# Kernel tuning notes

Measured on AMD Instinct MI355X. Metric: run time of the kernel, lower is better.

Reference implementation:

```python
import jax, jax.numpy as jnp
import numpy as np

SQ, SK, B, H, D = 2048, 2048, 2, 16, 64
LAYER_NUMBER = 1  # coeff for query_key_layer_scaling
MASK_FILL = -10000.0  # attention_mask_func fill value


def setup_inputs() -> dict:
    key = jax.random.key(0)
    kq, kk, kv = jax.random.split(key, 3)
    query_layer = jax.random.normal(kq, (SQ, B, H, D), dtype=jnp.float32)
    key_layer = jax.random.normal(kk, (SK, B, H, D), dtype=jnp.float32)
    value_layer = jax.random.normal(kv, (SK, B, H, D), dtype=jnp.float32)
    attention_mask = jnp.zeros((B, 1, SQ, SK), dtype=bool)  # ignored for causal mask type
    return {
        "query_layer": query_layer,
        "key_layer": key_layer,
        "value_layer": value_layer,
        "attention_mask": attention_mask,
    }


def reference(query_layer, key_layer, value_layer, attention_mask):
    sq, b, h, d = query_layer.shape
    sk = key_layer.shape[0]
    coeff = float(LAYER_NUMBER)
    norm_factor = np.sqrt(d) * coeff  # norm_factor = sqrt(d) * layer_number

    # BMM1: [b,h,sq,sk] scores, scaled by 1/norm_factor
    scores = jnp.einsum("sbhd,tbhd->bhst", query_layer, key_layer) / norm_factor

    # FusedScaleMaskSoftmax: scale by coeff in fp32, causal mask, softmax
    scores = scores.astype(jnp.float32) * coeff
    causal = jnp.triu(jnp.ones((sq, sk), dtype=bool), k=1)  # True above diagonal -> masked
    scores = jnp.where(causal[None, None], MASK_FILL, scores)
    probs = jax.nn.softmax(scores, axis=-1).astype(query_layer.dtype)

    # dropout p=0.0 -> identity

    # BMM2: context [sq,b,h,d] -> [sq,b,h*d]
    context = jnp.einsum("bhst,tbhd->sbhd", probs, value_layer)
    return context.reshape(sq, b, h * d)
```

## Files before the change

### kernel.cpp

```cpp
#include <hip/hip_runtime.h>

typedef short bf16x8 __attribute__((ext_vector_type(8)));
typedef float f32x4 __attribute__((ext_vector_type(4)));
typedef unsigned u32x4 __attribute__((ext_vector_type(4)));
typedef unsigned u32x2 __attribute__((ext_vector_type(2)));

#define RS 2048
#define LDSK 72
#define QSCALE 0.18033688011f

static __device__ __forceinline__ unsigned pkbf(float a, float b) {
    union { float f; unsigned u; } ua, ub; ua.f = a; ub.f = b;
    return ((ua.u + 0x8000u) >> 16) | ((ub.u + 0x8000u) & 0xffff0000u);
}

static __device__ __forceinline__ float fexp2(float x) {
#if __has_builtin(__builtin_amdgcn_exp2f)
    return __builtin_amdgcn_exp2f(x);
#else
    return exp2f(x);
#endif
}

__global__ __launch_bounds__(256, 2)
void fa_fwd(const float* __restrict__ Q, const float* __restrict__ K,
            const float* __restrict__ V, float* __restrict__ Out)
{
    __shared__ short Ksh[64 * LDSK];
    __shared__ short Vt[64 * LDSK];
    __shared__ short Psh[4][16 * LDSK];

    const int x = blockIdx.x;
    const int bh = blockIdx.y;
    const int base = bh * 64;
    const int tid = threadIdx.x;
    const int wave = tid >> 6, lane = tid & 63;
    const int n15 = lane & 15, quad = lane >> 4;

    const int tA = x;
    const int tB = 31 - x;

    const int krow = tid >> 2, kcg = (tid & 3) * 16;
    const int vkey = (tid & 31) * 2, vd = (tid >> 5) * 4;

    bf16x8 qfA[2], qfB[2];
    {
        const float* qa = Q + (size_t)(tA * 64 + wave * 16 + n15) * RS + base + quad * 8;
        const float* qb = Q + (size_t)(tB * 64 + wave * 16 + n15) * RS + base + quad * 8;
        #pragma unroll
        for (int ks = 0; ks < 2; ++ks) {
            f32x4 a0 = *(const f32x4*)(qa + ks * 32) * QSCALE;
            f32x4 a1 = *(const f32x4*)(qa + ks * 32 + 4) * QSCALE;
            union { u32x4 u; bf16x8 s; } wa;
            wa.u[0] = pkbf(a0[0], a0[1]); wa.u[1] = pkbf(a0[2], a0[3]);
            wa.u[2] = pkbf(a1[0], a1[1]); wa.u[3] = pkbf(a1[2], a1[3]);
            qfA[ks] = wa.s;
            f32x4 b0 = *(const f32x4*)(qb + ks * 32) * QSCALE;
            f32x4 b1 = *(const f32x4*)(qb + ks * 32 + 4) * QSCALE;
            union { u32x4 u; bf16x8 s; } wb;
            wb.u[0] = pkbf(b0[0], b0[1]); wb.u[1] = pkbf(b0[2], b0[3]);
            wb.u[2] = pkbf(b1[0], b1[1]); wb.u[3] = pkbf(b1[2], b1[3]);
            qfB[ks] = wb.s;
        }
    }

    f32x4 OA[4], OB[4];
    #pragma unroll
    for (int i = 0; i < 4; ++i) { OA[i] = (f32x4){0.f,0.f,0.f,0.f}; OB[i] = (f32x4){0.f,0.f,0.f,0.f}; }
    float lA = 0.f, lB = 0.f;

    f32x4 rk0, rk1, rk2, rk3, rv0, rv1, rv2, rv3;

    auto prefetch = [&](int kt) {
        const int kb = kt * 64;
        const float* kp = K + (size_t)(kb + krow) * RS + base + kcg;
        rk0 = *(const f32x4*)kp;       rk1 = *(const f32x4*)(kp + 4);
        rk2 = *(const f32x4*)(kp + 8); rk3 = *(const f32x4*)(kp + 12);
        const float* vp = V + (size_t)(kb + vkey) * RS + base + vd;
        rv0 = *(const f32x4*)vp;        rv1 = *(const f32x4*)(vp + RS);
        rv2 = *(const f32x4*)(vp + 32); rv3 = *(const f32x4*)(vp + RS + 32);
    };

    auto stage = [&]() {
        u32x4 w0; w0[0] = pkbf(rk0[0], rk0[1]); w0[1] = pkbf(rk0[2], rk0[3]);
                  w0[2] = pkbf(rk1[0], rk1[1]); w0[3] = pkbf(rk1[2], rk1[3]);
        *(u32x4*)&Ksh[krow * LDSK + kcg] = w0;
        u32x4 w1; w1[0] = pkbf(rk2[0], rk2[1]); w1[1] = pkbf(rk2[2], rk2[3]);
                  w1[2] = pkbf(rk3[0], rk3[1]); w1[3] = pkbf(rk3[2], rk3[3]);
        *(u32x4*)&Ksh[krow * LDSK + kcg + 8] = w1;
        #pragma unroll
        for (int i = 0; i < 4; ++i) {
            *(unsigned*)&Vt[(vd + i) * LDSK + vkey] = pkbf(rv0[i], rv1[i]);
            *(unsigned*)&Vt[(vd + 32 + i) * LDSK + vkey] = pkbf(rv2[i], rv3[i]);
        }
    };

    auto compute = [&](int tbase, int kb, bool diag, const bf16x8* qf, f32x4* O, float& l) {
        f32x4 S[4];
        #pragma unroll
        for (int mb = 0; mb < 4; ++mb) {
            f32x4 s = (f32x4){0.f,0.f,0.f,0.f};
            bf16x8 kf0 = *(const bf16x8*)&Ksh[(mb * 16 + n15) * LDSK + quad * 8];
            s = __builtin_amdgcn_mfma_f32_16x16x32_bf16(kf0, qf[0], s, 0, 0, 0);
            bf16x8 kf1 = *(const bf16x8*)&Ksh[(mb * 16 + n15) * LDSK + 32 + quad * 8];
            s = __builtin_amdgcn_mfma_f32_16x16x32_bf16(kf1, qf[1], s, 0, 0, 0);
            S[mb] = s;
        }
        if (diag) {
            int q = tbase + wave * 16 + n15;
            #pragma unroll
            for (int mb = 0; mb < 4; ++mb)
                #pragma unroll
                for (int r = 0; r < 4; ++r)
                    if (kb + mb * 16 + quad * 4 + r > q) S[mb][r] = -1e30f;
        }
        float rs = 0.f;
        #pragma unroll
        for (int mb = 0; mb < 4; ++mb) {
            float p0 = fexp2(S[mb][0]), p1 = fexp2(S[mb][1]);
            float p2 = fexp2(S[mb][2]), p3 = fexp2(S[mb][3]);
            rs += (p0 + p1) + (p2 + p3);
            u32x2 w; w[0] = pkbf(p0, p1); w[1] = pkbf(p2, p3);
            *(u32x2*)&Psh[wave][n15 * LDSK + mb * 16 + quad * 4] = w;
        }
        rs += __shfl_xor(rs, 16);
        rs += __shfl_xor(rs, 32);
        l += rs;
        bf16x8 pf0 = *(const bf16x8*)&Psh[wave][n15 * LDSK + quad * 8];
        bf16x8 pf1 = *(const bf16x8*)&Psh[wave][n15 * LDSK + 32 + quad * 8];
        #pragma unroll
        for (int db = 0; db < 4; ++db) {
            bf16x8 vf0 = *(const bf16x8*)&Vt[(db * 16 + n15) * LDSK + quad * 8];
            O[db] = __builtin_amdgcn_mfma_f32_16x16x32_bf16(pf0, vf0, O[db], 0, 0, 0);
            bf16x8 vf1 = *(const bf16x8*)&Vt[(db * 16 + n15) * LDSK + 32 + quad * 8];
            O[db] = __builtin_amdgcn_mfma_f32_16x16x32_bf16(pf1, vf1, O[db], 0, 0, 0);
        }
    };

    prefetch(0);
    const int ktmax = tB;
    for (int kt = 0; kt <= ktmax; ++kt) {
        __syncthreads();
        stage();
        __syncthreads();
        if (kt < ktmax) prefetch(kt + 1);
        compute(tB * 64, kt * 64, kt == tB, qfB, OB, lB);
        if (kt <= tA)
            compute(tA * 64, kt * 64, kt == tA, qfA, OA, lA);
    }

    #pragma unroll
    for (int r = 0; r < 4; ++r) {
        float invB = 1.0f / __shfl(lB, quad * 4 + r);
        size_t rowB = (size_t)(tB * 64 + wave * 16 + quad * 4 + r) * RS + base;
        #pragma unroll
        for (int db = 0; db < 4; ++db)
            Out[rowB + db * 16 + n15] = OB[db][r] * invB;
        float invA = 1.0f / __shfl(lA, quad * 4 + r);
        size_t rowA = (size_t)(tA * 64 + wave * 16 + quad * 4 + r) * RS + base;
        #pragma unroll
        for (int db = 0; db < 4; ++db)
            Out[rowA + db * 16 + n15] = OA[db][r] * invA;
    }
}

extern "C" void kernel_launch(void* const* d_in, const int* in_sizes, int n_in,
                              void* d_out, int out_size, void* d_ws, size_t ws_size,
                              hipStream_t stream) {
    const float* Q = (const float*)d_in[0];
    const float* K = (const float*)d_in[1];
    const float* V = (const float*)d_in[2];
    float* Out = (float*)d_out;
    dim3 grid(16, 32);
    fa_fwd<<<grid, dim3(256), 0, stream>>>(Q, K, V, Out);
}
```

Before: 165.8 us.

## Replace paired causal Q tiles with one tile per block and double-buffered K/V

```diff
diff --git a/kernel.cpp b/kernel.cpp
--- a/kernel.cpp
+++ b/kernel.cpp
@@ -14,60 +14,45 @@
     return ((ua.u + 0x8000u) >> 16) | ((ub.u + 0x8000u) & 0xffff0000u);
 }
 
-static __device__ __forceinline__ float fexp2(float x) {
-#if __has_builtin(__builtin_amdgcn_exp2f)
-    return __builtin_amdgcn_exp2f(x);
-#else
-    return exp2f(x);
-#endif
-}
+static __device__ __forceinline__ float fexp2(float x) { return exp2f(x); }
 
-__global__ __launch_bounds__(256, 2)
+__global__ __launch_bounds__(256, 3)
 void fa_fwd(const float* __restrict__ Q, const float* __restrict__ K,
             const float* __restrict__ V, float* __restrict__ Out)
 {
-    __shared__ short Ksh[64 * LDSK];
-    __shared__ short Vt[64 * LDSK];
+    __shared__ short Ksh[2][64 * LDSK];
+    __shared__ short Vt[2][64 * LDSK];
     __shared__ short Psh[4][16 * LDSK];
 
-    const int x = blockIdx.x;
-    const int bh = blockIdx.y;
+    const int qt = 31 - blockIdx.y;
+    const int bh = blockIdx.x;
     const int base = bh * 64;
     const int tid = threadIdx.x;
     const int wave = tid >> 6, lane = tid & 63;
     const int n15 = lane & 15, quad = lane >> 4;
-
-    const int tA = x;
-    const int tB = 31 - x;
+    const int q0 = qt * 64;
 
     const int krow = tid >> 2, kcg = (tid & 3) * 16;
     const int vkey = (tid & 31) * 2, vd = (tid >> 5) * 4;
 
-    bf16x8 qfA[2], qfB[2];
+    bf16x8 qf[2];
     {
-        const float* qa = Q + (size_t)(tA * 64 + wave * 16 + n15) * RS + base + quad * 8;
-        const float* qb = Q + (size_t)(tB * 64 + wave * 16 + n15) * RS + base + quad * 8;
+        const float* qp = Q + (size_t)(q0 + wave * 16 + n15) * RS + base + quad * 8;
         #pragma unroll
         for (int ks = 0; ks < 2; ++ks) {
-            f32x4 a0 = *(const f32x4*)(qa + ks * 32) * QSCALE;
-            f32x4 a1 = *(const f32x4*)(qa + ks * 32 + 4) * QSCALE;
-            union { u32x4 u; bf16x8 s; } wa;
-            wa.u[0] = pkbf(a0[0], a0[1]); wa.u[1] = pkbf(a0[2], a0[3]);
-            wa.u[2] = pkbf(a1[0], a1[1]); wa.u[3] = pkbf(a1[2], a1[3]);
-            qfA[ks] = wa.s;
-            f32x4 b0 = *(const f32x4*)(qb + ks * 32) * QSCALE;
-            f32x4 b1 = *(const f32x4*)(qb + ks * 32 + 4) * QSCALE;
-            union { u32x4 u; bf16x8 s; } wb;
-            wb.u[0] = pkbf(b0[0], b0[1]); wb.u[1] = pkbf(b0[2], b0[3]);
-            wb.u[2] = pkbf(b1[0], b1[1]); wb.u[3] = pkbf(b1[2], b1[3]);
-            qfB[ks] = wb.s;
+            f32x4 a0 = *(const f32x4*)(qp + ks * 32) * QSCALE;
+            f32x4 a1 = *(const f32x4*)(qp + ks * 32 + 4) * QSCALE;
+            union { u32x4 u; bf16x8 s; } w;
+            w.u[0] = pkbf(a0[0], a0[1]); w.u[1] = pkbf(a0[2], a0[3]);
+            w.u[2] = pkbf(a1[0], a1[1]); w.u[3] = pkbf(a1[2], a1[3]);
+            qf[ks] = w.s;
         }
     }
 
-    f32x4 OA[4], OB[4];
+    f32x4 O[4];
     #pragma unroll
-    for (int i = 0; i < 4; ++i) { OA[i] = (f32x4){0.f,0.f,0.f,0.f}; OB[i] = (f32x4){0.f,0.f,0.f,0.f}; }
-    float lA = 0.f, lB = 0.f;
+    for (int i = 0; i < 4; ++i) O[i] = (f32x4){0.f, 0.f, 0.f, 0.f};
+    float l = 0.f;
 
     f32x4 rk0, rk1, rk2, rk3, rv0, rv1, rv2, rv3;
 
@@ -81,33 +66,33 @@
         rv2 = *(const f32x4*)(vp + 32); rv3 = *(const f32x4*)(vp + RS + 32);
     };
 
-    auto stage = [&]() {
+    auto stage = [&](int buf) {
         u32x4 w0; w0[0] = pkbf(rk0[0], rk0[1]); w0[1] = pkbf(rk0[2], rk0[3]);
                   w0[2] = pkbf(rk1[0], rk1[1]); w0[3] = pkbf(rk1[2], rk1[3]);
-        *(u32x4*)&Ksh[krow * LDSK + kcg] = w0;
+        *(u32x4*)&Ksh[buf][krow * LDSK + kcg] = w0;
         u32x4 w1; w1[0] = pkbf(rk2[0], rk2[1]); w1[1] = pkbf(rk2[2], rk2[3]);
                   w1[2] = pkbf(rk3[0], rk3[1]); w1[3] = pkbf(rk3[2], rk3[3]);
-        *(u32x4*)&Ksh[krow * LDSK + kcg + 8] = w1;
+        *(u32x4*)&Ksh[buf][krow * LDSK + kcg + 8] = w1;
         #pragma unroll
         for (int i = 0; i < 4; ++i) {
-            *(unsigned*)&Vt[(vd + i) * LDSK + vkey] = pkbf(rv0[i], rv1[i]);
-            *(unsigned*)&Vt[(vd + 32 + i) * LDSK + vkey] = pkbf(rv2[i], rv3[i]);
+            *(unsigned*)&Vt[buf][(vd + i) * LDSK + vkey] = pkbf(rv0[i], rv1[i]);
+            *(unsigned*)&Vt[buf][(vd + 32 + i) * LDSK + vkey] = pkbf(rv2[i], rv3[i]);
         }
     };
 
-    auto compute = [&](int tbase, int kb, bool diag, const bf16x8* qf, f32x4* O, float& l) {
+    auto compute = [&](int buf, int kb, bool diag) {
         f32x4 S[4];
         #pragma unroll
         for (int mb = 0; mb < 4; ++mb) {
-            f32x4 s = (f32x4){0.f,0.f,0.f,0.f};
-            bf16x8 kf0 = *(const bf16x8*)&Ksh[(mb * 16 + n15) * LDSK + quad * 8];
+            f32x4 s = (f32x4){0.f, 0.f, 0.f, 0.f};
+            bf16x8 kf0 = *(const bf16x8*)&Ksh[buf][(mb * 16 + n15) * LDSK + quad * 8];
             s = __builtin_amdgcn_mfma_f32_16x16x32_bf16(kf0, qf[0], s, 0, 0, 0);
-            bf16x8 kf1 = *(const bf16x8*)&Ksh[(mb * 16 + n15) * LDSK + 32 + quad * 8];
+            bf16x8 kf1 = *(const bf16x8*)&Ksh[buf][(mb * 16 + n15) * LDSK + 32 + quad * 8];
             s = __builtin_amdgcn_mfma_f32_16x16x32_bf16(kf1, qf[1], s, 0, 0, 0);
             S[mb] = s;
         }
         if (diag) {
-            int q = tbase + wave * 16 + n15;
+            int q = q0 + wave * 16 + n15;
             #pragma unroll
             for (int mb = 0; mb < 4; ++mb)
                 #pragma unroll
@@ -130,37 +115,31 @@
         bf16x8 pf1 = *(const bf16x8*)&Psh[wave][n15 * LDSK + 32 + quad * 8];
         #pragma unroll
         for (int db = 0; db < 4; ++db) {
-            bf16x8 vf0 = *(const bf16x8*)&Vt[(db * 16 + n15) * LDSK + quad * 8];
+            bf16x8 vf0 = *(const bf16x8*)&Vt[buf][(db * 16 + n15) * LDSK + quad * 8];
             O[db] = __builtin_amdgcn_mfma_f32_16x16x32_bf16(pf0, vf0, O[db], 0, 0, 0);
-            bf16x8 vf1 = *(const bf16x8*)&Vt[(db * 16 + n15) * LDSK + 32 + quad * 8];
+            bf16x8 vf1 = *(const bf16x8*)&Vt[buf][(db * 16 + n15) * LDSK + 32 + quad * 8];
             O[db] = __builtin_amdgcn_mfma_f32_16x16x32_bf16(pf1, vf1, O[db], 0, 0, 0);
         }
     };
 
     prefetch(0);
-    const int ktmax = tB;
-    for (int kt = 0; kt <= ktmax; ++kt) {
+    stage(0);
+    __syncthreads();
+    for (int kt = 0; kt <= qt; ++kt) {
+        const int cur = kt & 1;
+        if (kt < qt) prefetch(kt + 1);
+        compute(cur, kt * 64, kt == qt);
+        if (kt < qt) stage(1 - cur);
         __syncthreads();
-        stage();
-        __syncthreads();
-        if (kt < ktmax) prefetch(kt + 1);
-        compute(tB * 64, kt * 64, kt == tB, qfB, OB, lB);
-        if (kt <= tA)
-            compute(tA * 64, kt * 64, kt == tA, qfA, OA, lA);
     }
 
     #pragma unroll
     for (int r = 0; r < 4; ++r) {
-        float invB = 1.0f / __shfl(lB, quad * 4 + r);
-        size_t rowB = (size_t)(tB * 64 + wave * 16 + quad * 4 + r) * RS + base;
+        float inv = 1.0f / __shfl(l, quad * 4 + r);
+        size_t row = (size_t)(q0 + wave * 16 + quad * 4 + r) * RS + base;
         #pragma unroll
         for (int db = 0; db < 4; ++db)
-            Out[rowB + db * 16 + n15] = OB[db][r] * invB;
-        float invA = 1.0f / __shfl(lA, quad * 4 + r);
-        size_t rowA = (size_t)(tA * 64 + wave * 16 + quad * 4 + r) * RS + base;
-        #pragma unroll
-        for (int db = 0; db < 4; ++db)
-            Out[rowA + db * 16 + n15] = OA[db][r] * invA;
+            Out[row + db * 16 + n15] = O[db][r] * inv;
     }
 }
 
@@ -171,6 +150,6 @@
     const float* K = (const float*)d_in[1];
     const float* V = (const float*)d_in[2];
     float* Out = (float*)d_out;
-    dim3 grid(16, 32);
+    dim3 grid(32, 32);
     fa_fwd<<<grid, dim3(256), 0, stream>>>(Q, K, V, Out);
 }
```

Result: faster. 160.4 us (-3.2%).
